# Performance work log

Hardware: AMD Instinct MI355X
Metric: run time of the kernel (lower is better)

## Reference

```python
import jax, jax.numpy as jnp
import numpy as np

D_MODEL = 1024
N_HEAD = 16
D_K = D_MODEL // N_HEAD


def setup_inputs() -> dict:
    key = jax.random.key(0)
    ks = jax.random.split(key, 11)
    B, T = 2, 2048
    s = 1.0 / np.sqrt(D_MODEL)
    return {
        "q": jax.random.normal(ks[0], (B, T, D_MODEL), jnp.float32),
        "k": jax.random.normal(ks[1], (B, T, D_MODEL), jnp.float32),
        "v": jax.random.normal(ks[2], (B, T, D_MODEL), jnp.float32),
        "w_q": jax.random.normal(ks[3], (D_MODEL, D_MODEL), jnp.float32) * s,
        "b_q": jax.random.normal(ks[4], (D_MODEL,), jnp.float32) * 0.01,
        "w_k": jax.random.normal(ks[5], (D_MODEL, D_MODEL), jnp.float32) * s,
        "b_k": jax.random.normal(ks[6], (D_MODEL,), jnp.float32) * 0.01,
        "w_v": jax.random.normal(ks[7], (D_MODEL, D_MODEL), jnp.float32) * s,
        "b_v": jax.random.normal(ks[8], (D_MODEL,), jnp.float32) * 0.01,
        "w_o": jax.random.normal(ks[9], (D_MODEL, D_MODEL), jnp.float32) * s,
        "b_o": jax.random.normal(ks[10], (D_MODEL,), jnp.float32) * 0.01,
    }


def reference(q, k, v, w_q, b_q, w_k, b_k, w_v, b_v, w_o, b_o):
    B, T, _ = q.shape
    # QKV projections -> [B, H, T, d_k]
    def proj(x, w, b):
        return (jnp.einsum('btd,de->bte', x, w) + b).reshape(B, T, N_HEAD, D_K).transpose(0, 2, 1, 3)
    qh = proj(q, w_q, b_q)
    kh = proj(k, w_k, b_k)
    vh = proj(v, w_v, b_v)
    scale = jnp.float32(1.0 / np.sqrt(D_K))
    scores = jnp.einsum('bhqd,bhkd->bhqk', qh, kh) * scale  # [B,H,T,T]
    attn = jax.nn.softmax(scores, axis=-1)
    # dropout is identity in eval mode
    out = jnp.einsum('bhqk,bhkd->bhqd', attn, vh)  # [B,H,T,d_k]
    out = out.transpose(0, 2, 1, 3).reshape(B, T, N_HEAD * D_K)
    return jnp.einsum('btd,de->bte', out, w_o) + b_o
```

## Files before the change

kernel.cpp:

```cpp
#include <hip/hip_runtime.h>
#include <stdint.h>

#define DEVI static __device__ __forceinline__

typedef float f32x4 __attribute__((ext_vector_type(4)));
typedef float f32x16 __attribute__((ext_vector_type(16)));
typedef short s16x8 __attribute__((ext_vector_type(8)));
typedef unsigned short u16x4 __attribute__((ext_vector_type(4)));
typedef uint32_t u32x2 __attribute__((ext_vector_type(2)));
typedef uint32_t u32x4 __attribute__((ext_vector_type(4)));

DEVI unsigned short f2bf(float f) {
  union { float f; uint32_t u; } v; v.f = f;
  uint32_t u = v.u;
  return (unsigned short)((u + 0x7fffu + ((u >> 16) & 1u)) >> 16);
}

DEVI float bf2f(unsigned short u) {
  union { uint32_t u; float f; } v;
  v.u = ((uint32_t)u) << 16;
  return v.f;
}

DEVI uint32_t cvtpk(float lo, float hi) {
  uint32_t r;
  asm("v_cvt_pk_bf16_f32 %0, %1, %2" : "=v"(r) : "v"(lo), "v"(hi));
  return r;
}

DEVI float fexp2(float x) {
#if __has_builtin(__builtin_amdgcn_exp2f)
  return __builtin_amdgcn_exp2f(x);
#else
  return exp2f(x);
#endif
}

DEVI void pl32swap(uint32_t& a, uint32_t& b) {
#if __has_builtin(__builtin_amdgcn_permlane32_swap)
  u32x2 r = __builtin_amdgcn_permlane32_swap(a, b, false, false);
  a = r[0]; b = r[1];
#else
  asm("v_permlane32_swap_b32 %0, %1" : "+v"(a), "+v"(b));
#endif
}

DEVI float swap_half(float x, int hi) {
  uint32_t a = __float_as_uint(x), b = a;
  pl32swap(a, b);
  return hi ? __uint_as_float(a) : __uint_as_float(b);
}

DEVI void g2l16(const void* g, void* l) {
  __builtin_amdgcn_global_load_lds(
      (const __attribute__((address_space(1))) void*)g,
      (__attribute__((address_space(3))) void*)l, 16, 0, 0);
}

DEVI float vmax16(const f32x16& v) {
  float a = fmaxf(fmaxf(v[0], v[1]), fmaxf(v[2], v[3]));
  float b = fmaxf(fmaxf(v[4], v[5]), fmaxf(v[6], v[7]));
  float c = fmaxf(fmaxf(v[8], v[9]), fmaxf(v[10], v[11]));
  float d = fmaxf(fmaxf(v[12], v[13]), fmaxf(v[14], v[15]));
  return fmaxf(fmaxf(a, b), fmaxf(c, d));
}

DEVI float vsum16(const f32x16& v) {
  float a = (v[0] + v[1]) + (v[2] + v[3]);
  float b = (v[4] + v[5]) + (v[6] + v[7]);
  float c = (v[8] + v[9]) + (v[10] + v[11]);
  float d = (v[12] + v[13]) + (v[14] + v[15]);
  return (a + b) + (c + d);
}

__global__ __launch_bounds__(256) void k_cvt3(const float* __restrict__ q,
                                              const float* __restrict__ k,
                                              const float* __restrict__ v,
                                              unsigned short* __restrict__ out) {
  const int y = blockIdx.y;
  const float* in = y == 0 ? q : y == 1 ? k : v;
  unsigned short* o = out + (size_t)y * 4194304;
  int idx = blockIdx.x * blockDim.x + threadIdx.x;
  int stride = gridDim.x * blockDim.x;
  for (int i = idx * 4; i < 4194304; i += stride * 4) {
    f32x4 x = *(const f32x4*)(in + i);
    u16x4 r;
    for (int j = 0; j < 4; ++j) r[j] = f2bf(x[j]);
    *(u16x4*)(o + i) = r;
  }
}

__global__ __launch_bounds__(256) void k_wt4(const float* w0, const float* w1,
                                             const float* w2, const float* w3,
                                             unsigned short* t0, unsigned short* t1,
                                             unsigned short* t2, unsigned short* t3) {
  const int z = blockIdx.z;
  const float* w = z == 0 ? w0 : z == 1 ? w1 : z == 2 ? w2 : w3;
  unsigned short* wt = z == 0 ? t0 : z == 1 ? t1 : z == 2 ? t2 : t3;
  __shared__ float tile[32][33];
  const int tx = threadIdx.x, ty = threadIdx.y;
  const int n0 = blockIdx.x * 32, k0 = blockIdx.y * 32;
  for (int j = 0; j < 4; ++j)
    tile[ty + j * 8][tx] = w[(size_t)(k0 + ty + j * 8) * 1024 + n0 + tx];
  __syncthreads();
  for (int j = 0; j < 4; ++j)
    wt[(size_t)(n0 + ty + j * 8) * 1024 + k0 + tx] = f2bf(tile[tx][ty + j * 8]);
}

__global__ __launch_bounds__(256) void k_gemm_multi(
    const unsigned short* A0, const unsigned short* A1, const unsigned short* A2,
    const unsigned short* B0, const unsigned short* B1, const unsigned short* B2,
    const float* c0, const float* c1, const float* c2,
    void* o0, void* o1, void* o2, int mode0) {
  constexpr int K = 1024;
  const int z = blockIdx.y;
  const unsigned short* A = z == 0 ? A0 : z == 1 ? A1 : A2;
  const unsigned short* Bt = z == 0 ? B0 : z == 1 ? B1 : B2;
  const float* bias = z == 0 ? c0 : z == 1 ? c1 : c2;
  void* outp = z == 0 ? o0 : z == 1 ? o1 : o2;
  const int MODE = mode0 + z;

  __shared__ __align__(16) unsigned short As[128 * 64];
  __shared__ __align__(16) unsigned short Bs[64 * 64];
  const int tid = threadIdx.x;
  const int lane = tid & 63, w = tid >> 6;
  const int g = lane >> 4, c = lane & 15;
  const int wgid = (blockIdx.x & 7) * 64 + (blockIdx.x >> 3);
  const int bm = wgid >> 4, bn = wgid & 15;
  const int m0 = bm * 128, n0 = bn * 64;
  const int wr = w >> 1, wc = w & 1;
  f32x4 acc[4][2] = {};

  for (int kt = 0; kt < 16; ++kt) {
    const int k0 = kt * 64;
    __syncthreads();
#pragma unroll
    for (int it = 0; it < 4; ++it) {
      int e = it * 256 + tid;
      int row = e >> 3, cwp = (e & 7) ^ (row & 7);
      g2l16(A + (size_t)(m0 + row) * K + k0 + cwp * 8,
            (char*)As + (it * 256 + (w << 6)) * 16);
    }
#pragma unroll
    for (int it = 0; it < 2; ++it) {
      int e = it * 256 + tid;
      int row = e >> 3, cwp = (e & 7) ^ (row & 7);
      g2l16(Bt + (size_t)(n0 + row) * K + k0 + cwp * 8,
            (char*)Bs + (it * 256 + (w << 6)) * 16);
    }
    __syncthreads();
    for (int kk = 0; kk < 2; ++kk) {
      s16x8 af[4], bfr[2];
      for (int mi = 0; mi < 4; ++mi) {
        int row = wr * 64 + mi * 16 + c;
        int ch = (kk * 4 + g) ^ (row & 7);
        af[mi] = *(const s16x8*)((const char*)As + row * 128 + ch * 16);
      }
      for (int ni = 0; ni < 2; ++ni) {
        int row = wc * 32 + ni * 16 + c;
        int ch = (kk * 4 + g) ^ (row & 7);
        bfr[ni] = *(const s16x8*)((const char*)Bs + row * 128 + ch * 16);
      }
      for (int mi = 0; mi < 4; ++mi)
        for (int ni = 0; ni < 2; ++ni)
          acc[mi][ni] = __builtin_amdgcn_mfma_f32_16x16x32_bf16(
              af[mi], bfr[ni], acc[mi][ni], 0, 0, 0);
    }
  }

  if (MODE == 0 || MODE == 1) {
    unsigned short* out = (unsigned short*)outp;
    const float scale = (MODE == 0) ? 0.1803368801111204f : 1.0f;
    for (int mi = 0; mi < 4; ++mi)
      for (int ni = 0; ni < 2; ++ni) {
        int row = m0 + wr * 64 + mi * 16 + g * 4;
        int col = n0 + wc * 32 + ni * 16 + c;
        float bb = bias[col];
        for (int r = 0; r < 4; ++r)
          out[(size_t)(row + r) * 1024 + col] = f2bf((acc[mi][ni][r] + bb) * scale);
      }
  } else if (MODE == 2) {
    unsigned short* vt = (unsigned short*)outp;
    const int bq = m0 >> 11, t0 = m0 & 2047;
    for (int mi = 0; mi < 4; ++mi)
      for (int ni = 0; ni < 2; ++ni) {
        int rowb = wr * 64 + mi * 16 + g * 4;
        int coll = wc * 32 + ni * 16 + c;
        float bb = bias[n0 + coll];
        u16x4 pk;
        for (int r = 0; r < 4; ++r) pk[r] = f2bf(acc[mi][ni][r] + bb);
        *(u16x4*)(vt + (size_t)(bq * 1024 + n0 + coll) * 2048 + t0 + rowb) = pk;
      }
  } else {
    float* out = (float*)outp;
    for (int mi = 0; mi < 4; ++mi)
      for (int ni = 0; ni < 2; ++ni) {
        int row = m0 + wr * 64 + mi * 16 + g * 4;
        int col = n0 + wc * 32 + ni * 16 + c;
        float bb = bias[col];
        for (int r = 0; r < 4; ++r)
          out[(size_t)(row + r) * 1024 + col] = acc[mi][ni][r] + bb;
      }
  }
}

__global__ __launch_bounds__(256) void k_attn(const unsigned short* __restrict__ Qp,
                                              const unsigned short* __restrict__ Kp,
                                              const unsigned short* __restrict__ Vt,
                                              unsigned short* __restrict__ Po0,
                                              unsigned short* __restrict__ Po1,
                                              float2* __restrict__ ml) {
  __shared__ __align__(16) unsigned short Ks[2][4096];
  __shared__ __align__(16) unsigned short Vs[2][4096];
  const int tid = threadIdx.x;
  const int lane = tid & 63, w = tid >> 6;
  const int l31 = lane & 31, hi = lane >> 5;
  const int blk = (blockIdx.x & 7) * 128 + (blockIdx.x >> 3);
  const int half = blk & 1, qt = (blk >> 1) & 15, bh = blk >> 5;
  const int b = bh >> 4, h = bh & 15;
  const int m0 = qt * 128 + w * 32;
  const size_t qkBase = (size_t)b * 2048 * 1024 + (size_t)h * 64;
  const size_t vtBase = ((size_t)b * 1024 + h * 64) * 2048;

  const unsigned short* qrow = Qp + qkBase + (size_t)(m0 + l31) * 1024;
  s16x8 bq[4];
#pragma unroll
  for (int s = 0; s < 4; ++s)
    bq[s] = *(const s16x8*)(qrow + s * 16 + hi * 8);

  const int srow = tid >> 2, c4 = tid & 3;
  const unsigned short* kg = Kp + qkBase + (size_t)srow * 1024 + c4 * 16 +
                             (size_t)half * 1048576;
  const unsigned short* vg = Vt + vtBase + (size_t)srow * 2048 + c4 * 16 +
                             half * 1024;
  int wof[2];
#pragma unroll
  for (int j = 0; j < 2; ++j)
    wof[j] = srow * 128 + (((c4 * 2 + j) ^ (srow & 7)) * 16);

  float m_run = -1e30f, l_run = 0.f;
  f32x16 o0 = {}, o1 = {};

  {
    s16x8 k0 = *(const s16x8*)(kg), k1 = *(const s16x8*)(kg + 8);
    s16x8 v0 = *(const s16x8*)(vg), v1 = *(const s16x8*)(vg + 8);
    *(s16x8*)((char*)&Ks[0][0] + wof[0]) = k0;
    *(s16x8*)((char*)&Ks[0][0] + wof[1]) = k1;
    *(s16x8*)((char*)&Vs[0][0] + wof[0]) = v0;
    *(s16x8*)((char*)&Vs[0][0] + wof[1]) = v1;
  }
  __syncthreads();

  const int rch = l31 & 7;

#pragma unroll 1
  for (int t = 0; t < 16; ++t) {
    const int cur = t & 1;
    s16x8 k0, k1, v0, v1;
    if (t < 15) {
      const unsigned short* kgt = kg + (size_t)(t + 1) * 65536;
      const unsigned short* vgt = vg + (t + 1) * 64;
      k0 = *(const s16x8*)(kgt); k1 = *(const s16x8*)(kgt + 8);
      v0 = *(const s16x8*)(vgt); v1 = *(const s16x8*)(vgt + 8);
    }
    const char* ks = (const char*)&Ks[cur][0];
    const char* vs = (const char*)&Vs[cur][0];

    f32x16 s0 = {}, s1 = {};
    __builtin_amdgcn_s_setprio(1);
#pragma unroll
    for (int ds = 0; ds < 4; ++ds) {
      int ch = (2 * ds + hi) ^ rch;
      s16x8 a0 = *(const s16x8*)(ks + l31 * 128 + ch * 16);
      s16x8 a1 = *(const s16x8*)(ks + (32 + l31) * 128 + ch * 16);
      s0 = __builtin_amdgcn_mfma_f32_32x32x16_bf16(a0, bq[ds], s0, 0, 0, 0);
      s1 = __builtin_amdgcn_mfma_f32_32x32x16_bf16(a1, bq[ds], s1, 0, 0, 0);
    }
    __builtin_amdgcn_s_setprio(0);

    float tm = fmaxf(vmax16(s0), vmax16(s1));
    tm = fmaxf(tm, swap_half(tm, hi));
    if (!__all(tm - m_run <= 8.0f)) {
      float mt = fmaxf(m_run, tm);
      float al = fexp2(m_run - mt);
      l_run *= al;
#pragma unroll
      for (int j = 0; j < 16; ++j) { o0[j] *= al; o1[j] *= al; }
      m_run = mt;
    }
#pragma unroll
    for (int j = 0; j < 16; ++j) s0[j] = fexp2(s0[j] - m_run);
#pragma unroll
    for (int j = 0; j < 16; ++j) s1[j] = fexp2(s1[j] - m_run);
    l_run += vsum16(s0) + vsum16(s1);

    s16x8 pf[4];
    {
      uint32_t w0 = cvtpk(s0[0], s0[1]), w1 = cvtpk(s0[2], s0[3]);
      uint32_t w2 = cvtpk(s0[4], s0[5]), w3 = cvtpk(s0[6], s0[7]);
      uint32_t w4 = cvtpk(s0[8], s0[9]), w5 = cvtpk(s0[10], s0[11]);
      uint32_t w6 = cvtpk(s0[12], s0[13]), w7 = cvtpk(s0[14], s0[15]);
      pl32swap(w0, w2); pl32swap(w1, w3); pl32swap(w4, w6); pl32swap(w5, w7);
      u32x4 f0 = {w0, w1, w2, w3}, f1 = {w4, w5, w6, w7};
      pf[0] = *(s16x8*)&f0;
      pf[1] = *(s16x8*)&f1;
    }
    {
      uint32_t w0 = cvtpk(s1[0], s1[1]), w1 = cvtpk(s1[2], s1[3]);
      uint32_t w2 = cvtpk(s1[4], s1[5]), w3 = cvtpk(s1[6], s1[7]);
      uint32_t w4 = cvtpk(s1[8], s1[9]), w5 = cvtpk(s1[10], s1[11]);
      uint32_t w6 = cvtpk(s1[12], s1[13]), w7 = cvtpk(s1[14], s1[15]);
      pl32swap(w0, w2); pl32swap(w1, w3); pl32swap(w4, w6); pl32swap(w5, w7);
      u32x4 f0 = {w0, w1, w2, w3}, f1 = {w4, w5, w6, w7};
      pf[2] = *(s16x8*)&f0;
      pf[3] = *(s16x8*)&f1;
    }

    __builtin_amdgcn_s_setprio(1);
#pragma unroll
    for (int ksp = 0; ksp < 4; ++ksp) {
      int ch = (2 * ksp + hi) ^ rch;
      s16x8 a0 = *(const s16x8*)(vs + l31 * 128 + ch * 16);
      s16x8 a1 = *(const s16x8*)(vs + (32 + l31) * 128 + ch * 16);
      o0 = __builtin_amdgcn_mfma_f32_32x32x16_bf16(a0, pf[ksp], o0, 0, 0, 0);
      o1 = __builtin_amdgcn_mfma_f32_32x32x16_bf16(a1, pf[ksp], o1, 0, 0, 0);
    }
    __builtin_amdgcn_s_setprio(0);

    if (t < 15) {
      const int nb = cur ^ 1;
      *(s16x8*)((char*)&Ks[nb][0] + wof[0]) = k0;
      *(s16x8*)((char*)&Ks[nb][0] + wof[1]) = k1;
      *(s16x8*)((char*)&Vs[nb][0] + wof[0]) = v0;
      *(s16x8*)((char*)&Vs[nb][0] + wof[1]) = v1;
    }
    __syncthreads();
  }

  float lt = l_run + swap_half(l_run, hi);
  float inv = 1.0f / lt;
  unsigned short* Po = half ? Po1 : Po0;
  unsigned short* arow = Po + ((size_t)b * 2048 + m0 + l31) * 1024 + h * 64;
#pragma unroll
  for (int dblk = 0; dblk < 2; ++dblk) {
#pragma unroll
    for (int rq = 0; rq < 4; ++rq) {
      float e0 = (dblk ? o1[rq * 4 + 0] : o0[rq * 4 + 0]) * inv;
      float e1 = (dblk ? o1[rq * 4 + 1] : o0[rq * 4 + 1]) * inv;
      float e2 = (dblk ? o1[rq * 4 + 2] : o0[rq * 4 + 2]) * inv;
      float e3 = (dblk ? o1[rq * 4 + 3] : o0[rq * 4 + 3]) * inv;
      u32x2 pk;
      pk[0] = cvtpk(e0, e1);
      pk[1] = cvtpk(e2, e3);
      *(u32x2*)(arow + dblk * 32 + 8 * rq + 4 * hi) = pk;
    }
  }
  if (hi == 0) {
    int qid = ((b << 4) + h) * 2048 + m0 + l31;
    ml[half * 65536 + qid] = {m_run, lt};
  }
}

__global__ __launch_bounds__(256) void k_comb(const unsigned short* __restrict__ Po0,
                                              const unsigned short* __restrict__ Po1,
                                              const float2* __restrict__ ml,
                                              unsigned short* __restrict__ Att) {
  int idx = blockIdx.x * 256 + threadIdx.x;
  int base = idx * 8;
  int qrow = base >> 10, col = base & 1023;
  int h = col >> 6, b = qrow >> 11, t = qrow & 2047;
  int qid = ((b << 4) + h) * 2048 + t;
  float2 p0 = ml[qid], p1 = ml[65536 + qid];
  float ms = fmaxf(p0.x, p1.x);
  float a0 = fexp2(p0.x - ms) * p0.y, a1 = fexp2(p1.x - ms) * p1.y;
  float inv = 1.0f / (a0 + a1);
  float w0 = a0 * inv, w1 = a1 * inv;
  s16x8 v0 = *(const s16x8*)(Po0 + base);
  s16x8 v1 = *(const s16x8*)(Po1 + base);
  u32x4 pk;
#pragma unroll
  for (int j = 0; j < 4; ++j) {
    float e0 = w0 * bf2f((unsigned short)v0[2 * j]) + w1 * bf2f((unsigned short)v1[2 * j]);
    float e1 = w0 * bf2f((unsigned short)v0[2 * j + 1]) + w1 * bf2f((unsigned short)v1[2 * j + 1]);
    pk[j] = cvtpk(e0, e1);
  }
  *(u32x4*)(Att + base) = pk;
}

extern "C" void kernel_launch(void* const* d_in, const int* in_sizes, int n_in,
                              void* d_out, int out_size, void* d_ws, size_t ws_size,
                              hipStream_t stream) {
  const float* q = (const float*)d_in[0];
  const float* k = (const float*)d_in[1];
  const float* v = (const float*)d_in[2];
  const float* w_q = (const float*)d_in[3];
  const float* b_q = (const float*)d_in[4];
  const float* w_k = (const float*)d_in[5];
  const float* b_k = (const float*)d_in[6];
  const float* w_v = (const float*)d_in[7];
  const float* b_v = (const float*)d_in[8];
  const float* w_o = (const float*)d_in[9];
  const float* b_o = (const float*)d_in[10];

  unsigned short* s = (unsigned short*)d_ws;
  unsigned short* qbf = s;
  unsigned short* kbf = s + 4194304;
  unsigned short* vbf = s + 8388608;
  unsigned short* wqT = s + 12582912;
  unsigned short* wkT = s + 13631488;
  unsigned short* wvT = s + 14680064;
  unsigned short* woT = s + 15728640;
  unsigned short* Qp  = s + 16777216;
  unsigned short* Kp  = s + 20971520;
  unsigned short* Vt  = s + 25165824;
  unsigned short* Po0 = qbf;
  unsigned short* Po1 = kbf;
  unsigned short* Att = vbf;
  float2* ml = (float2*)wqT;

  k_cvt3<<<dim3(1024, 3), 256, 0, stream>>>(q, k, v, qbf);

  k_wt4<<<dim3(32, 32, 4), dim3(32, 8), 0, stream>>>(w_q, w_k, w_v, w_o,
                                                     wqT, wkT, wvT, woT);

  k_gemm_multi<<<dim3(512, 3), 256, 0, stream>>>(
      qbf, kbf, vbf, wqT, wkT, wvT, b_q, b_k, b_v,
      (void*)Qp, (void*)Kp, (void*)Vt, 0);

  k_attn<<<1024, 256, 0, stream>>>(Qp, Kp, Vt, Po0, Po1, ml);

  k_comb<<<2048, 256, 0, stream>>>(Po0, Po1, ml, Att);

  k_gemm_multi<<<dim3(512, 1), 256, 0, stream>>>(
      Att, Att, Att, woT, woT, woT, b_o, b_o, b_o,
      d_out, d_out, d_out, 3);
}
```

Baseline: 134.7 us.

## Split attention KV into four chunks, merge prep kernels, use max3

The attention kernel now splits the key/value sequence four ways instead of two, launching 2048 blocks, each looping over 8 KV tiles. The combine kernel merges four partial outputs using their max/sum statistics. The convert and transpose prep kernels are fused into one launch, and the row max uses v_max3. The goal is more parallelism per head and less launch overhead, at the cost of extra partial-output traffic and a heavier combine step.

```diff
diff --git a/kernel.cpp b/kernel.cpp
--- a/kernel.cpp
+++ b/kernel.cpp
@@ -34,6 +34,12 @@
 #else
   return exp2f(x);
 #endif
+}
+
+DEVI float max3(float a, float b, float c) {
+  float r;
+  asm("v_max3_f32 %0, %1, %2, %3" : "=v"(r) : "v"(a), "v"(b), "v"(c));
+  return r;
 }
 
 DEVI void pl32swap(uint32_t& a, uint32_t& b) {
@@ -58,11 +64,14 @@
 }
 
 DEVI float vmax16(const f32x16& v) {
-  float a = fmaxf(fmaxf(v[0], v[1]), fmaxf(v[2], v[3]));
-  float b = fmaxf(fmaxf(v[4], v[5]), fmaxf(v[6], v[7]));
-  float c = fmaxf(fmaxf(v[8], v[9]), fmaxf(v[10], v[11]));
-  float d = fmaxf(fmaxf(v[12], v[13]), fmaxf(v[14], v[15]));
-  return fmaxf(fmaxf(a, b), fmaxf(c, d));
+  float a = max3(v[0], v[1], v[2]);
+  float b = max3(v[3], v[4], v[5]);
+  float c = max3(v[6], v[7], v[8]);
+  float d = max3(v[9], v[10], v[11]);
+  float e = max3(v[12], v[13], v[14]);
+  float x = max3(a, b, c);
+  float y = max3(d, e, v[15]);
+  return fmaxf(x, y);
 }
 
 DEVI float vsum16(const f32x16& v) {
@@ -73,38 +82,39 @@
   return (a + b) + (c + d);
 }
 
-__global__ __launch_bounds__(256) void k_cvt3(const float* __restrict__ q,
-                                              const float* __restrict__ k,
-                                              const float* __restrict__ v,
-                                              unsigned short* __restrict__ out) {
-  const int y = blockIdx.y;
-  const float* in = y == 0 ? q : y == 1 ? k : v;
-  unsigned short* o = out + (size_t)y * 4194304;
-  int idx = blockIdx.x * blockDim.x + threadIdx.x;
-  int stride = gridDim.x * blockDim.x;
-  for (int i = idx * 4; i < 4194304; i += stride * 4) {
-    f32x4 x = *(const f32x4*)(in + i);
-    u16x4 r;
-    for (int j = 0; j < 4; ++j) r[j] = f2bf(x[j]);
-    *(u16x4*)(o + i) = r;
-  }
-}
-
-__global__ __launch_bounds__(256) void k_wt4(const float* w0, const float* w1,
-                                             const float* w2, const float* w3,
-                                             unsigned short* t0, unsigned short* t1,
-                                             unsigned short* t2, unsigned short* t3) {
-  const int z = blockIdx.z;
-  const float* w = z == 0 ? w0 : z == 1 ? w1 : z == 2 ? w2 : w3;
-  unsigned short* wt = z == 0 ? t0 : z == 1 ? t1 : z == 2 ? t2 : t3;
+__global__ __launch_bounds__(256) void k_prep(
+    const float* __restrict__ q, const float* __restrict__ k,
+    const float* __restrict__ v, unsigned short* __restrict__ qkv,
+    const float* __restrict__ w0, const float* __restrict__ w1,
+    const float* __restrict__ w2, const float* __restrict__ w3,
+    unsigned short* __restrict__ t0, unsigned short* __restrict__ t1,
+    unsigned short* __restrict__ t2, unsigned short* __restrict__ t3) {
   __shared__ float tile[32][33];
-  const int tx = threadIdx.x, ty = threadIdx.y;
-  const int n0 = blockIdx.x * 32, k0 = blockIdx.y * 32;
-  for (int j = 0; j < 4; ++j)
-    tile[ty + j * 8][tx] = w[(size_t)(k0 + ty + j * 8) * 1024 + n0 + tx];
-  __syncthreads();
-  for (int j = 0; j < 4; ++j)
-    wt[(size_t)(n0 + ty + j * 8) * 1024 + k0 + tx] = f2bf(tile[tx][ty + j * 8]);
+  const int bx = blockIdx.x;
+  if (bx < 3072) {
+    const int y = bx >> 10;
+    const float* in = y == 0 ? q : y == 1 ? k : v;
+    unsigned short* o = qkv + (size_t)y * 4194304;
+    int idx = (bx & 1023) * 256 + threadIdx.x;
+    for (int i = idx * 4; i < 4194304; i += 1048576) {
+      f32x4 x = *(const f32x4*)(in + i);
+      u16x4 r;
+      for (int j = 0; j < 4; ++j) r[j] = f2bf(x[j]);
+      *(u16x4*)(o + i) = r;
+    }
+  } else {
+    const int wb = bx - 3072;
+    const int z = wb >> 10, tb = wb & 1023;
+    const float* w = z == 0 ? w0 : z == 1 ? w1 : z == 2 ? w2 : w3;
+    unsigned short* wt = z == 0 ? t0 : z == 1 ? t1 : z == 2 ? t2 : t3;
+    const int n0 = (tb & 31) * 32, k0 = (tb >> 5) * 32;
+    const int tx = threadIdx.x & 31, ty = threadIdx.x >> 5;
+    for (int j = 0; j < 4; ++j)
+      tile[ty + j * 8][tx] = w[(size_t)(k0 + ty + j * 8) * 1024 + n0 + tx];
+    __syncthreads();
+    for (int j = 0; j < 4; ++j)
+      wt[(size_t)(n0 + ty + j * 8) * 1024 + k0 + tx] = f2bf(tile[tx][ty + j * 8]);
+  }
 }
 
 __global__ __launch_bounds__(256) void k_gemm_multi(
@@ -209,14 +219,16 @@
                                               const unsigned short* __restrict__ Vt,
                                               unsigned short* __restrict__ Po0,
                                               unsigned short* __restrict__ Po1,
+                                              unsigned short* __restrict__ Po2,
+                                              unsigned short* __restrict__ Po3,
                                               float2* __restrict__ ml) {
   __shared__ __align__(16) unsigned short Ks[2][4096];
   __shared__ __align__(16) unsigned short Vs[2][4096];
   const int tid = threadIdx.x;
   const int lane = tid & 63, w = tid >> 6;
   const int l31 = lane & 31, hi = lane >> 5;
-  const int blk = (blockIdx.x & 7) * 128 + (blockIdx.x >> 3);
-  const int half = blk & 1, qt = (blk >> 1) & 15, bh = blk >> 5;
+  const int blk = (blockIdx.x & 7) * 256 + (blockIdx.x >> 3);
+  const int sp = blk & 3, qt = (blk >> 2) & 15, bh = blk >> 6;
   const int b = bh >> 4, h = bh & 15;
   const int m0 = qt * 128 + w * 32;
   const size_t qkBase = (size_t)b * 2048 * 1024 + (size_t)h * 64;
@@ -230,9 +242,9 @@
 
   const int srow = tid >> 2, c4 = tid & 3;
   const unsigned short* kg = Kp + qkBase + (size_t)srow * 1024 + c4 * 16 +
-                             (size_t)half * 1048576;
+                             (size_t)sp * 524288;
   const unsigned short* vg = Vt + vtBase + (size_t)srow * 2048 + c4 * 16 +
-                             half * 1024;
+                             sp * 512;
   int wof[2];
 #pragma unroll
   for (int j = 0; j < 2; ++j)
@@ -254,10 +266,10 @@
   const int rch = l31 & 7;
 
 #pragma unroll 1
-  for (int t = 0; t < 16; ++t) {
+  for (int t = 0; t < 8; ++t) {
     const int cur = t & 1;
     s16x8 k0, k1, v0, v1;
-    if (t < 15) {
+    if (t < 7) {
       const unsigned short* kgt = kg + (size_t)(t + 1) * 65536;
       const unsigned short* vgt = vg + (t + 1) * 64;
       k0 = *(const s16x8*)(kgt); k1 = *(const s16x8*)(kgt + 8);
@@ -327,7 +339,7 @@
     }
     __builtin_amdgcn_s_setprio(0);
 
-    if (t < 15) {
+    if (t < 7) {
       const int nb = cur ^ 1;
       *(s16x8*)((char*)&Ks[nb][0] + wof[0]) = k0;
       *(s16x8*)((char*)&Ks[nb][0] + wof[1]) = k1;
@@ -339,7 +351,7 @@
 
   float lt = l_run + swap_half(l_run, hi);
   float inv = 1.0f / lt;
-  unsigned short* Po = half ? Po1 : Po0;
+  unsigned short* Po = sp == 0 ? Po0 : sp == 1 ? Po1 : sp == 2 ? Po2 : Po3;
   unsigned short* arow = Po + ((size_t)b * 2048 + m0 + l31) * 1024 + h * 64;
 #pragma unroll
   for (int dblk = 0; dblk < 2; ++dblk) {
@@ -357,12 +369,14 @@
   }
   if (hi == 0) {
     int qid = ((b << 4) + h) * 2048 + m0 + l31;
-    ml[half * 65536 + qid] = {m_run, lt};
+    ml[sp * 65536 + qid] = {m_run, lt};
   }
 }
 
 __global__ __launch_bounds__(256) void k_comb(const unsigned short* __restrict__ Po0,
                                               const unsigned short* __restrict__ Po1,
+                                              const unsigned short* __restrict__ Po2,
+                                              const unsigned short* __restrict__ Po3,
                                               const float2* __restrict__ ml,
                                               unsigned short* __restrict__ Att) {
   int idx = blockIdx.x * 256 + threadIdx.x;
@@ -371,17 +385,23 @@
   int h = col >> 6, b = qrow >> 11, t = qrow & 2047;
   int qid = ((b << 4) + h) * 2048 + t;
   float2 p0 = ml[qid], p1 = ml[65536 + qid];
-  float ms = fmaxf(p0.x, p1.x);
+  float2 p2 = ml[131072 + qid], p3 = ml[196608 + qid];
+  float ms = fmaxf(fmaxf(p0.x, p1.x), fmaxf(p2.x, p3.x));
   float a0 = fexp2(p0.x - ms) * p0.y, a1 = fexp2(p1.x - ms) * p1.y;
-  float inv = 1.0f / (a0 + a1);
-  float w0 = a0 * inv, w1 = a1 * inv;
+  float a2 = fexp2(p2.x - ms) * p2.y, a3 = fexp2(p3.x - ms) * p3.y;
+  float inv = 1.0f / ((a0 + a1) + (a2 + a3));
+  float w0 = a0 * inv, w1 = a1 * inv, w2 = a2 * inv, w3 = a3 * inv;
   s16x8 v0 = *(const s16x8*)(Po0 + base);
   s16x8 v1 = *(const s16x8*)(Po1 + base);
+  s16x8 v2 = *(const s16x8*)(Po2 + base);
+  s16x8 v3 = *(const s16x8*)(Po3 + base);
   u32x4 pk;
 #pragma unroll
   for (int j = 0; j < 4; ++j) {
-    float e0 = w0 * bf2f((unsigned short)v0[2 * j]) + w1 * bf2f((unsigned short)v1[2 * j]);
-    float e1 = w0 * bf2f((unsigned short)v0[2 * j + 1]) + w1 * bf2f((unsigned short)v1[2 * j + 1]);
+    float e0 = w0 * bf2f((unsigned short)v0[2 * j]) + w1 * bf2f((unsigned short)v1[2 * j]) +
+               w2 * bf2f((unsigned short)v2[2 * j]) + w3 * bf2f((unsigned short)v3[2 * j]);
+    float e1 = w0 * bf2f((unsigned short)v0[2 * j + 1]) + w1 * bf2f((unsigned short)v1[2 * j + 1]) +
+               w2 * bf2f((unsigned short)v2[2 * j + 1]) + w3 * bf2f((unsigned short)v3[2 * j + 1]);
     pk[j] = cvtpk(e0, e1);
   }
   *(u32x4*)(Att + base) = pk;
@@ -413,23 +433,23 @@
   unsigned short* Qp  = s + 16777216;
   unsigned short* Kp  = s + 20971520;
   unsigned short* Vt  = s + 25165824;
+  unsigned short* Po3 = s + 29360128;
   unsigned short* Po0 = qbf;
   unsigned short* Po1 = kbf;
-  unsigned short* Att = vbf;
+  unsigned short* Po2 = vbf;
+  unsigned short* Att = Qp;
   float2* ml = (float2*)wqT;
 
-  k_cvt3<<<dim3(1024, 3), 256, 0, stream>>>(q, k, v, qbf);
-
-  k_wt4<<<dim3(32, 32, 4), dim3(32, 8), 0, stream>>>(w_q, w_k, w_v, w_o,
-                                                     wqT, wkT, wvT, woT);
+  k_prep<<<7168, 256, 0, stream>>>(q, k, v, qbf, w_q, w_k, w_v, w_o,
+                                   wqT, wkT, wvT, woT);
 
   k_gemm_multi<<<dim3(512, 3), 256, 0, stream>>>(
       qbf, kbf, vbf, wqT, wkT, wvT, b_q, b_k, b_v,
       (void*)Qp, (void*)Kp, (void*)Vt, 0);
 
-  k_attn<<<1024, 256, 0, stream>>>(Qp, Kp, Vt, Po0, Po1, ml);
-
-  k_comb<<<2048, 256, 0, stream>>>(Po0, Po1, ml, Att);
+  k_attn<<<2048, 256, 0, stream>>>(Qp, Kp, Vt, Po0, Po1, Po2, Po3, ml);
+
+  k_comb<<<2048, 256, 0, stream>>>(Po0, Po1, Po2, Po3, ml, Att);
 
   k_gemm_multi<<<dim3(512, 1), 256, 0, stream>>>(
       Att, Att, Att, woT, woT, woT, b_o, b_o, b_o,
```

New measurement: 137.5 us. 2.1% more time.
